# Kernel tuning notes

Measured on AMD Instinct MI355X. Metric: run time of the kernel, lower is better.

The kernel has to match this reference:

```python
import jax, jax.numpy as jnp
import numpy as np
import math

B, C, F, W, NH = 2, 8, 1024, 512, 8
HD = F // NH


def conv2d(x, w, b):
    # NCHW 3x3 same-padding conv with bias
    y = jax.lax.conv_general_dilated(x, w, (1, 1), [(1, 1), (1, 1)],
                                     dimension_numbers=('NCHW', 'OIHW', 'NCHW'))
    return y + b[None, :, None, None]


def mc_linear(x, w):
    # per-channel linear over the feature (h) axis: (b,c,h,w) x (c,f,h) -> (b,c,f,w)
    return jnp.einsum('bchw,cfh->bcfw', x, w)


def split_heads(t):
    # (b,c,f,w) -> transpose(2,3) -> (b,c,w,f) -> (b,c,w,nh,hd) -> (b,c,nh,w,hd)
    b, c, f, w = t.shape
    return jnp.transpose(t.transpose(0, 1, 3, 2).reshape(b, c, w, NH, HD), (0, 1, 3, 2, 4))


def rotate_queries_or_keys(x):
    # lucidrains-style interleaved rotary over the sequence axis (dim -2)
    d, w = x.shape[-1], x.shape[-2]
    inv_freq = 1.0 / (10000.0 ** (jnp.arange(0, d, 2, dtype=jnp.float32) / d))
    freqs = jnp.arange(w, dtype=jnp.float32)[:, None] * inv_freq[None, :]  # (w, d/2)
    freqs = jnp.repeat(freqs, 2, axis=-1)  # (w, d)
    cos, sin = jnp.cos(freqs), jnp.sin(freqs)
    xp = x.reshape(*x.shape[:-1], d // 2, 2)
    x1, x2 = xp[..., 0], xp[..., 1]
    x_rot = jnp.stack((-x2, x1), axis=-1).reshape(x.shape)
    return x * cos + x_rot * sin


def _forward(x, prev_qk, wq_conv, bq_conv, wq_lin, wk_conv, bk_conv, wk_lin,
             wv_conv, bv_conv, wv_lin, wo_lin):
    b, c, h, w = x.shape
    q = rotate_queries_or_keys(split_heads(mc_linear(conv2d(x, wq_conv, bq_conv), wq_lin)))
    k = rotate_queries_or_keys(split_heads(mc_linear(conv2d(x, wk_conv, bk_conv), wk_lin)))
    v = split_heads(mc_linear(conv2d(x, wv_conv, bv_conv), wv_lin))
    # NOTE: original scales by sqrt(h) == sqrt(features), not sqrt(head_dim)
    qk = jnp.einsum('bcnqd,bcnkd->bcnqk', q, k) / math.sqrt(h) + prev_qk
    a = jnp.einsum('bcnqk,bcnkd->bcnqd', jax.nn.softmax(qk, axis=-1), v)
    a = jnp.transpose(a, (0, 1, 3, 2, 4)).reshape(b, c, w, h).transpose(0, 1, 3, 2)
    out = mc_linear(a, wo_lin)
    return out, qk


def setup_inputs() -> dict:
    key = jax.random.key(0)
    ks = jax.random.split(key, 10)
    s = 0.02
    return {
        'x': jax.random.normal(ks[0], (B, C, F, W), dtype=jnp.float32),
        'prev_qk': jax.random.normal(ks[1], (B, C, NH, W, W), dtype=jnp.float32) * 0.1,
        'wq_conv': jax.random.normal(ks[2], (C, C, 3, 3), dtype=jnp.float32) * s,
        'bq_conv': jnp.zeros((C,), dtype=jnp.float32),
        'wq_lin': jax.random.normal(ks[3], (C, F, F), dtype=jnp.float32) * s,
        'wk_conv': jax.random.normal(ks[4], (C, C, 3, 3), dtype=jnp.float32) * s,
        'bk_conv': jnp.zeros((C,), dtype=jnp.float32),
        'wk_lin': jax.random.normal(ks[5], (C, F, F), dtype=jnp.float32) * s,
        'wv_conv': jax.random.normal(ks[6], (C, C, 3, 3), dtype=jnp.float32) * s,
        'bv_conv': jnp.zeros((C,), dtype=jnp.float32),
        'wv_lin': jax.random.normal(ks[7], (C, F, F), dtype=jnp.float32) * s,
        'wo_lin': jax.random.normal(ks[8], (C, F, F), dtype=jnp.float32) * s,
    }


def reference(x, prev_qk, wq_conv, bq_conv, wq_lin, wk_conv, bk_conv, wk_lin,
              wv_conv, bv_conv, wv_lin, wo_lin):
    return _forward(x, prev_qk, wq_conv, bq_conv, wq_lin, wk_conv, bk_conv, wk_lin,
                    wv_conv, bv_conv, wv_lin, wo_lin)
```

## Files before the change

kernel.cpp:

```cpp
#include <hip/hip_runtime.h>
#include <stdint.h>


typedef float f32x4 __attribute__((ext_vector_type(4)));
typedef short s16x8 __attribute__((ext_vector_type(8)));

__device__ __forceinline__ short f2bf(float f) {
  union { float f; uint32_t u; } v; v.f = f;
  uint32_t r = v.u + 0x7FFFu + ((v.u >> 16) & 1u);
  return (short)(r >> 16);
}

__device__ __forceinline__ void g2l16(const void* g, void* l) {
  __builtin_amdgcn_global_load_lds(
      (const __attribute__((address_space(1))) void*)g,
      (__attribute__((address_space(3))) void*)l, 16, 0, 0);
}

__device__ __forceinline__ void gemm_core(const short* __restrict__ A,
                                          const short* __restrict__ B,
                                          int K, short* sA, short* sB,
                                          f32x4 (*acc)[4]) {
  const int tid = threadIdx.x;
  const int lane = tid & 63;
  const int wv = tid >> 6;
  const int wm = wv >> 1, wn = wv & 1;
  const int q = lane >> 4, cix = lane & 15;

  for (int k0 = 0; k0 < K; k0 += 32) {
    __syncthreads();
#pragma unroll
    for (int i = 0; i < 2; ++i) {
      int seg = wv + 4 * i;
      int m = seg * 16 + (lane >> 2);
      int ko = (lane & 3) * 8;
      g2l16(B + (size_t)m * K + k0 + ko, sB + seg * 512);
    }
#pragma unroll
    for (int i = 0; i < 2; ++i) {
      int seg = wv + 4 * i;
      int m = seg * 16 + (lane >> 2);
      int ko = (lane & 3) * 8;
      g2l16(A + (size_t)m * K + k0 + ko, sA + seg * 512);
    }
    __syncthreads();
    s16x8 afr[4], bfr[4];
#pragma unroll
    for (int i = 0; i < 4; ++i)
      afr[i] = *(const s16x8*)(sA + (wm * 64 + i * 16 + cix) * 32 + q * 8);
#pragma unroll
    for (int i = 0; i < 4; ++i)
      bfr[i] = *(const s16x8*)(sB + (wn * 64 + i * 16 + cix) * 32 + q * 8);
#pragma unroll
    for (int i = 0; i < 4; ++i)
#pragma unroll
      for (int j = 0; j < 4; ++j)
        acc[i][j] = __builtin_amdgcn_mfma_f32_16x16x32_bf16(afr[i], bfr[j],
                                                            acc[i][j], 0, 0, 0);
  }
}

__global__ void __launch_bounds__(256) k_cvt(
    const float* __restrict__ w0, const float* __restrict__ w1,
    const float* __restrict__ w2, const float* __restrict__ w3,
    short* __restrict__ Wb) {
  size_t i = (size_t)blockIdx.x * 256 + threadIdx.x;
#pragma unroll
  for (int r = 0; r < 4; ++r) {
    const float* s = (r == 0) ? w0 : (r == 1) ? w1 : (r == 2) ? w2 : w3;
    size_t v = i + (size_t)r * 2097152;
    float4 f = *(const float4*)(s + (i << 2));
    short4 o;
    o.x = f2bf(f.x); o.y = f2bf(f.y); o.z = f2bf(f.z); o.w = f2bf(f.w);
    *(short4*)(Wb + (v << 2)) = o;
  }
}

__global__ void __launch_bounds__(256) k_conv(
    const float* __restrict__ x,
    const float* __restrict__ wqc, const float* __restrict__ bqc,
    const float* __restrict__ wkc, const float* __restrict__ bkc,
    const float* __restrict__ wvc, const float* __restrict__ bvc,
    short* __restrict__ Yt) {
  __shared__ float xs[8][66][19];
  const int h0 = blockIdx.x * 64, w0 = blockIdx.y * 16, b = blockIdx.z;
  const int tid = threadIdx.x;
  for (int idx = tid; idx < 8 * 66 * 18; idx += 256) {
    int c = idx / (66 * 18);
    int rem = idx % (66 * 18);
    int r = rem / 18, cc = rem % 18;
    int h = h0 + r - 1, w = w0 + cc - 1;
    float v = 0.f;
    if (h >= 0 && h < 1024 && w >= 0 && w < 512)
      v = x[(((size_t)b * 8 + c) << 10 | (unsigned)h) * 512 + w];
    xs[c][r][cc] = v;
  }
  __syncthreads();
  const int hh = tid & 63;
  const int wv4 = tid >> 6;
  const size_t hgl = h0 + hh;
  for (int proj = 0; proj < 3; ++proj) {
    const float* wc = (proj == 0) ? wqc : ((proj == 1) ? wkc : wvc);
    const float* bc = (proj == 0) ? bqc : ((proj == 1) ? bkc : bvc);
    float a[4][8];
#pragma unroll
    for (int jj = 0; jj < 4; ++jj)
#pragma unroll
      for (int co = 0; co < 8; ++co) a[jj][co] = bc[co];
    for (int ci = 0; ci < 8; ++ci)
#pragma unroll
      for (int dh = 0; dh < 3; ++dh)
#pragma unroll
        for (int dw = 0; dw < 3; ++dw) {
          float xv[4];
#pragma unroll
          for (int jj = 0; jj < 4; ++jj)
            xv[jj] = xs[ci][hh + dh][wv4 * 4 + jj + dw];
          const int wi = ci * 9 + dh * 3 + dw;
#pragma unroll
          for (int co = 0; co < 8; ++co) {
            float wgt = wc[co * 72 + wi];
#pragma unroll
            for (int jj = 0; jj < 4; ++jj) a[jj][co] = fmaf(xv[jj], wgt, a[jj][co]);
          }
        }
#pragma unroll
    for (int jj = 0; jj < 4; ++jj) {
      size_t col = (size_t)b * 512 + w0 + wv4 * 4 + jj;
#pragma unroll
      for (int co = 0; co < 8; ++co)
        Yt[((size_t)(proj * 8 + co) << 20) + (col << 10) + hgl] = f2bf(a[jj][co]);
    }
  }
}

__global__ void __launch_bounds__(256) k_qkv(
    const short* __restrict__ Wb, const short* __restrict__ Yt,
    short* __restrict__ Qr, short* __restrict__ Kr, short* __restrict__ Vt) {
  __shared__ short sA[128 * 32], sB[128 * 32];
  const int L = blockIdx.x;
  const int lin = (L & 7) * 192 + (L >> 3);
  const int g = lin >> 6;
  const int t = lin & 63;
  const int proj = g >> 3, cq = g & 7;
  const int mt = t >> 3, nt = t & 7;
  const short* A = Wb + ((size_t)g << 20) + ((size_t)mt << 17);
  const short* B = Yt + ((size_t)g << 20) + ((size_t)nt << 17);
  const f32x4 fzero = {0.f, 0.f, 0.f, 0.f};
  f32x4 acc[4][4];
#pragma unroll
  for (int i = 0; i < 4; ++i)
#pragma unroll
    for (int j = 0; j < 4; ++j) acc[i][j] = fzero;
  gemm_core(A, B, 1024, sA, sB, acc);

  const int lane = threadIdx.x & 63, wv = threadIdx.x >> 6;
  const int wm = wv >> 1, wn = wv & 1, q = lane >> 4, cix = lane & 15;
  const int head = mt;
  if (proj == 2) {
#pragma unroll
    for (int mi = 0; mi < 4; ++mi) {
      int rbase = wm * 64 + mi * 16 + q * 4;
#pragma unroll
      for (int ni = 0; ni < 4; ++ni) {
        int col = nt * 128 + wn * 64 + ni * 16 + cix;
        int b = col >> 9, wpos = col & 511;
        size_t base = ((size_t)((cq * 8 + head) * 2 + b) << 16) +
                      ((size_t)rbase << 9) + wpos;
        f32x4 v = acc[mi][ni];
        Vt[base] = f2bf(v[0]);
        Vt[base + 512] = f2bf(v[1]);
        Vt[base + 1024] = f2bf(v[2]);
        Vt[base + 1536] = f2bf(v[3]);
      }
    }
  } else {
    short* QKp = proj ? Kr : Qr;
#pragma unroll
    for (int mi = 0; mi < 4; ++mi) {
      int rbase = wm * 64 + mi * 16 + q * 4;
      int j0 = rbase >> 1;
      float if0 = exp2f(-0.20762050593046f * (float)j0);
      float if1 = exp2f(-0.20762050593046f * (float)(j0 + 1));
#pragma unroll
      for (int ni = 0; ni < 4; ++ni) {
        int col = nt * 128 + wn * 64 + ni * 16 + cix;
        int b = col >> 9, wpos = col & 511;
        float fw = (float)wpos;
        float s0, c0, s1, c1;
        __sincosf(fw * if0, &s0, &c0);
        __sincosf(fw * if1, &s1, &c1);
        f32x4 v = acc[mi][ni];
        short4 pk;
        pk.x = f2bf(v[0] * c0 - v[1] * s0);
        pk.y = f2bf(v[1] * c0 + v[0] * s0);
        pk.z = f2bf(v[2] * c1 - v[3] * s1);
        pk.w = f2bf(v[3] * c1 + v[2] * s1);
        *(short4*)&QKp[((size_t)(((cq * 8 + head) * 2 + b) * 512 + wpos) << 7) +
                       rbase] = pk;
      }
    }
  }
}

__global__ void __launch_bounds__(256, 2) k_attn(
    const short* __restrict__ Qr, const short* __restrict__ Kr,
    const short* __restrict__ Vt, const float* __restrict__ prevqk,
    float* __restrict__ qk, short* __restrict__ At) {
  __shared__ short Qs[128 * 128];
  __shared__ short Pt[128 * 136];
  __shared__ float psum[128][2];
  const int tid = threadIdx.x, lane = tid & 63, wv = tid >> 6;
  const int wm = wv >> 1, wn = wv & 1, q = lane >> 4, cix = lane & 15;
  const int qt = blockIdx.x, bcn = blockIdx.y;
  const int b = bcn >> 6, cch = (bcn >> 3) & 7, nh = bcn & 7;
  const size_t qrb = ((size_t)((cch * 8 + nh) * 2 + b)) << 16;
  const size_t rowg0 = (size_t)bcn * 512 + qt * 128;
  const int arow = wm * 64;

  {
    const char* Qg = (const char*)(Qr + qrb + ((size_t)qt << 14));
#pragma unroll
    for (int i = 0; i < 8; ++i) {
      int Lb = i * 4096 + wv * 1024;
      int L = Lb + (lane << 4);
      int src = (L & ~255) | ((L & 255) ^ (((L >> 8) & 15) << 4));
      g2l16(Qg + src, (char*)Qs + Lb);
    }
  }
  __syncthreads();

  const f32x4 fzero = {0.f, 0.f, 0.f, 0.f};
  f32x4 accO[4][4];
  float lsum[4][4];
#pragma unroll
  for (int i = 0; i < 4; ++i)
#pragma unroll
    for (int j = 0; j < 4; ++j) { accO[i][j] = fzero; lsum[i][j] = 0.f; }

  float pvA[16], pvB[16];

#pragma unroll 1
  for (int kt = 0; kt < 4; ++kt) {
    const int colb = kt * 128 + wn * 64 + cix;
    f32x4 accS[4][4];
#pragma unroll
    for (int i = 0; i < 4; ++i)
#pragma unroll
      for (int j = 0; j < 4; ++j) accS[i][j] = fzero;

#pragma unroll
    for (int ni = 0; ni < 4; ++ni)
#pragma unroll
      for (int r = 0; r < 4; ++r)
        pvA[ni * 4 + r] =
            prevqk[((rowg0 + arow + q * 4 + r) << 9) + colb + ni * 16];

    const short* Kbase = Kr + qrb + ((size_t)kt << 14);
#pragma unroll
    for (int kk = 0; kk < 4; ++kk) {
      s16x8 afr[4], bfr[4];
      const int cb = kk * 64 + q * 16;
#pragma unroll
      for (int ni = 0; ni < 4; ++ni)
        bfr[ni] = *(const s16x8*)(Kbase +
            ((size_t)(wn * 64 + ni * 16 + cix) << 7) + kk * 32 + q * 8);
#pragma unroll
      for (int mi = 0; mi < 4; ++mi) {
        const int row = arow + mi * 16 + cix;
        afr[mi] = *(const s16x8*)((const char*)Qs + row * 256 +
                                  (cb ^ ((row & 15) << 4)));
      }
#pragma unroll
      for (int mi = 0; mi < 4; ++mi)
#pragma unroll
        for (int ni = 0; ni < 4; ++ni)
          accS[mi][ni] = __builtin_amdgcn_mfma_f32_16x16x32_bf16(
              afr[mi], bfr[ni], accS[mi][ni], 0, 0, 0);
    }

    auto ldchunk = [&](int mi, float* dst) {
#pragma unroll
      for (int ni = 0; ni < 4; ++ni)
#pragma unroll
        for (int r = 0; r < 4; ++r)
          dst[ni * 4 + r] =
              prevqk[((rowg0 + arow + mi * 16 + q * 4 + r) << 9) +
                     colb + ni * 16];
    };
    auto process = [&](int mi, const float* pv) {
      float rs[4] = {0.f, 0.f, 0.f, 0.f};
#pragma unroll
      for (int ni = 0; ni < 4; ++ni)
#pragma unroll
        for (int r = 0; r < 4; ++r) {
          float s = accS[mi][ni][r] * 0.03125f + pv[ni * 4 + r];
          qk[((rowg0 + arow + mi * 16 + q * 4 + r) << 9) + colb + ni * 16] = s;
          float p = __expf(s);
          rs[r] += p;
          Pt[(arow + mi * 16 + q * 4 + r) * 136 + wn * 64 + ni * 16 + cix] =
              f2bf(p);
        }
#pragma unroll
      for (int r = 0; r < 4; ++r) lsum[mi][r] += rs[r];
    };
    ldchunk(1, pvB);
    process(0, pvA);
    ldchunk(2, pvA);
    process(1, pvB);
    ldchunk(3, pvB);
    process(2, pvA);
    process(3, pvB);

    __syncthreads();

#pragma unroll
    for (int s4 = 0; s4 < 4; ++s4) {
      s16x8 afr[4], bfr[4];
#pragma unroll
      for (int i = 0; i < 4; ++i)
        afr[i] =
            *(const s16x8*)&Pt[(arow + i * 16 + cix) * 136 + s4 * 32 + q * 8];
#pragma unroll
      for (int i = 0; i < 4; ++i)
        bfr[i] = *(const s16x8*)&Vt[qrb +
                                    ((size_t)(wn * 64 + i * 16 + cix) << 9) +
                                    kt * 128 + s4 * 32 + q * 8];
#pragma unroll
      for (int i = 0; i < 4; ++i)
#pragma unroll
        for (int j = 0; j < 4; ++j)
          accO[i][j] = __builtin_amdgcn_mfma_f32_16x16x32_bf16(
              afr[i], bfr[j], accO[i][j], 0, 0, 0);
    }
    __syncthreads();
  }

#pragma unroll
  for (int mi = 0; mi < 4; ++mi)
#pragma unroll
    for (int r = 0; r < 4; ++r) {
      float se = lsum[mi][r];
      se += __shfl_xor(se, 1);
      se += __shfl_xor(se, 2);
      se += __shfl_xor(se, 4);
      se += __shfl_xor(se, 8);
      if (cix == 0) psum[arow + mi * 16 + q * 4 + r][wn] = se;
    }
  __syncthreads();
#pragma unroll
  for (int mi = 0; mi < 4; ++mi) {
    int rl = arow + mi * 16 + q * 4;
    float iL[4];
#pragma unroll
    for (int r = 0; r < 4; ++r)
      iL[r] = 1.0f / (psum[rl + r][0] + psum[rl + r][1]);
    int wq = qt * 128 + rl;
#pragma unroll
    for (int ni = 0; ni < 4; ++ni) {
      int dl = wn * 64 + ni * 16 + cix;
      size_t ob = (((size_t)cch << 10) + b * 512 + wq) * 1024 + nh * 128 + dl;
      f32x4 v = accO[mi][ni];
      At[ob] = f2bf(v[0] * iL[0]);
      At[ob + 1024] = f2bf(v[1] * iL[1]);
      At[ob + 2048] = f2bf(v[2] * iL[2]);
      At[ob + 3072] = f2bf(v[3] * iL[3]);
    }
  }
}

__global__ void __launch_bounds__(256) k_out(
    const short* __restrict__ At, const short* __restrict__ Wob,
    float* __restrict__ outp) {
  __shared__ short sA[128 * 32], sB[128 * 32];
  const int L = blockIdx.x;
  const int lin = (L & 7) * 64 + (L >> 3);
  const int c = lin >> 6;
  const int t = lin & 63;
  const int mt = t >> 3, nt = t & 7;
  const short* A = At + ((size_t)c << 20) + ((size_t)mt << 17);
  const short* B = Wob + ((size_t)c << 20) + ((size_t)nt << 17);
  const f32x4 fzero = {0.f, 0.f, 0.f, 0.f};
  f32x4 acc[4][4];
#pragma unroll
  for (int i = 0; i < 4; ++i)
#pragma unroll
    for (int j = 0; j < 4; ++j) acc[i][j] = fzero;
  gemm_core(A, B, 1024, sA, sB, acc);

  const int lane = threadIdx.x & 63, wv = threadIdx.x >> 6;
  const int wm = wv >> 1, wn = wv & 1, q = lane >> 4, cix = lane & 15;
#pragma unroll
  for (int mi = 0; mi < 4; ++mi) {
    int colm = mt * 128 + wm * 64 + mi * 16 + q * 4;
    int b = colm >> 9, w = colm & 511;
#pragma unroll
    for (int ni = 0; ni < 4; ++ni) {
      int f = nt * 128 + wn * 64 + ni * 16 + cix;
      f32x4 v = acc[mi][ni];
      float4 st; st.x = v[0]; st.y = v[1]; st.z = v[2]; st.w = v[3];
      *(float4*)&outp[((((size_t)b * 8 + c) << 10) + f) * 512 + w] = st;
    }
  }
}

extern "C" void kernel_launch(void* const* d_in, const int* in_sizes, int n_in,
                              void* d_out, int out_size, void* d_ws,
                              size_t ws_size, hipStream_t stream) {
  const float* x = (const float*)d_in[0];
  const float* prevqk = (const float*)d_in[1];
  const float* wqc = (const float*)d_in[2];
  const float* bqc = (const float*)d_in[3];
  const float* wql = (const float*)d_in[4];
  const float* wkc = (const float*)d_in[5];
  const float* bkc = (const float*)d_in[6];
  const float* wkl = (const float*)d_in[7];
  const float* wvc = (const float*)d_in[8];
  const float* bvc = (const float*)d_in[9];
  const float* wvl = (const float*)d_in[10];
  const float* wol = (const float*)d_in[11];
  float* outp = (float*)d_out;
  float* qk = outp + 8388608;

  char* ws = (char*)d_ws;
  short* Wb = (short*)ws;
  short* Yt = (short*)(ws + 67108864);
  short* Qr = (short*)(ws + 117440512);
  short* Kr = (short*)(ws + 134217728);
  short* Vt = (short*)(ws + 150994944);
  short* At = (short*)(ws + 67108864);
  short* Wob = Wb + ((size_t)24 << 20);

  k_cvt<<<dim3(8192), 256, 0, stream>>>(wql, wkl, wvl, wol, Wb);
  k_conv<<<dim3(16, 32, 2), 256, 0, stream>>>(x, wqc, bqc, wkc, bkc, wvc, bvc, Yt);
  k_qkv<<<dim3(1536), 256, 0, stream>>>(Wb, Yt, Qr, Kr, Vt);
  k_attn<<<dim3(4, 128), 256, 0, stream>>>(Qr, Kr, Vt, prevqk, qk, At);
  k_out<<<dim3(512), 256, 0, stream>>>(At, Wob, outp);
}
```

Measured before the change: 581.9 us.

## Drop Q LDS staging in attention, raise occupancy, remap blocks, interleave loads

The attention kernel stops staging the Q tile in shared memory and reads Q fragments straight from global memory. This cuts LDS use so the launch bound can ask for three blocks per CU instead of two. The grid becomes 1D with a swizzled block-to-(head, q-tile) mapping, and prev_qk prefetch buffers shrink to half-chunks issued ahead of the first QK MMA. It also interleaves K and V fragment loads with MFMAs under raised s_setprio. The trade-off is more global traffic for Q, which is reread per kt iteration and per wave, in exchange for higher occupancy and lower register pressure.

```diff
diff --git a/kernel.cpp b/kernel.cpp
--- a/kernel.cpp
+++ b/kernel.cpp
@@ -203,32 +203,22 @@
   }
 }
 
-__global__ void __launch_bounds__(256, 2) k_attn(
+__global__ void __launch_bounds__(256, 3) k_attn(
     const short* __restrict__ Qr, const short* __restrict__ Kr,
     const short* __restrict__ Vt, const float* __restrict__ prevqk,
     float* __restrict__ qk, short* __restrict__ At) {
-  __shared__ short Qs[128 * 128];
   __shared__ short Pt[128 * 136];
   __shared__ float psum[128][2];
   const int tid = threadIdx.x, lane = tid & 63, wv = tid >> 6;
   const int wm = wv >> 1, wn = wv & 1, q = lane >> 4, cix = lane & 15;
-  const int qt = blockIdx.x, bcn = blockIdx.y;
+  const int bid = blockIdx.x;
+  const int lin = (bid & 7) * 64 + (bid >> 3);
+  const int bcn = lin >> 2, qt = lin & 3;
   const int b = bcn >> 6, cch = (bcn >> 3) & 7, nh = bcn & 7;
   const size_t qrb = ((size_t)((cch * 8 + nh) * 2 + b)) << 16;
   const size_t rowg0 = (size_t)bcn * 512 + qt * 128;
   const int arow = wm * 64;
-
-  {
-    const char* Qg = (const char*)(Qr + qrb + ((size_t)qt << 14));
-#pragma unroll
-    for (int i = 0; i < 8; ++i) {
-      int Lb = i * 4096 + wv * 1024;
-      int L = Lb + (lane << 4);
-      int src = (L & ~255) | ((L & 255) ^ (((L >> 8) & 15) << 4));
-      g2l16(Qg + src, (char*)Qs + Lb);
-    }
-  }
-  __syncthreads();
+  const short* Qbase = Qr + qrb + ((size_t)qt << 14);
 
   const f32x4 fzero = {0.f, 0.f, 0.f, 0.f};
   f32x4 accO[4][4];
@@ -238,7 +228,7 @@
 #pragma unroll
     for (int j = 0; j < 4; ++j) { accO[i][j] = fzero; lsum[i][j] = 0.f; }
 
-  float pvA[16], pvB[16];
+  float pvA[8], pvB[8];
 
 #pragma unroll 1
   for (int kt = 0; kt < 4; ++kt) {
@@ -249,89 +239,84 @@
 #pragma unroll
       for (int j = 0; j < 4; ++j) accS[i][j] = fzero;
 
-#pragma unroll
-    for (int ni = 0; ni < 4; ++ni)
-#pragma unroll
-      for (int r = 0; r < 4; ++r)
-        pvA[ni * 4 + r] =
-            prevqk[((rowg0 + arow + q * 4 + r) << 9) + colb + ni * 16];
-
-    const short* Kbase = Kr + qrb + ((size_t)kt << 14);
-#pragma unroll
-    for (int kk = 0; kk < 4; ++kk) {
-      s16x8 afr[4], bfr[4];
-      const int cb = kk * 64 + q * 16;
-#pragma unroll
-      for (int ni = 0; ni < 4; ++ni)
-        bfr[ni] = *(const s16x8*)(Kbase +
-            ((size_t)(wn * 64 + ni * 16 + cix) << 7) + kk * 32 + q * 8);
-#pragma unroll
-      for (int mi = 0; mi < 4; ++mi) {
-        const int row = arow + mi * 16 + cix;
-        afr[mi] = *(const s16x8*)((const char*)Qs + row * 256 +
-                                  (cb ^ ((row & 15) << 4)));
-      }
-#pragma unroll
-      for (int mi = 0; mi < 4; ++mi)
-#pragma unroll
-        for (int ni = 0; ni < 4; ++ni)
-          accS[mi][ni] = __builtin_amdgcn_mfma_f32_16x16x32_bf16(
-              afr[mi], bfr[ni], accS[mi][ni], 0, 0, 0);
-    }
-
-    auto ldchunk = [&](int mi, float* dst) {
-#pragma unroll
-      for (int ni = 0; ni < 4; ++ni)
+    auto ld8 = [&](int mi, int h, float* dst) {
+#pragma unroll
+      for (int u = 0; u < 2; ++u)
 #pragma unroll
         for (int r = 0; r < 4; ++r)
-          dst[ni * 4 + r] =
+          dst[u * 4 + r] =
               prevqk[((rowg0 + arow + mi * 16 + q * 4 + r) << 9) +
-                     colb + ni * 16];
+                     colb + (2 * h + u) * 16];
     };
-    auto process = [&](int mi, const float* pv) {
-      float rs[4] = {0.f, 0.f, 0.f, 0.f};
-#pragma unroll
-      for (int ni = 0; ni < 4; ++ni)
+    auto pr8 = [&](int mi, int h, const float* pv) {
+#pragma unroll
+      for (int u = 0; u < 2; ++u) {
+        int ni = 2 * h + u;
 #pragma unroll
         for (int r = 0; r < 4; ++r) {
-          float s = accS[mi][ni][r] * 0.03125f + pv[ni * 4 + r];
+          float s = accS[mi][ni][r] * 0.03125f + pv[u * 4 + r];
           qk[((rowg0 + arow + mi * 16 + q * 4 + r) << 9) + colb + ni * 16] = s;
           float p = __expf(s);
-          rs[r] += p;
+          lsum[mi][r] += p;
           Pt[(arow + mi * 16 + q * 4 + r) * 136 + wn * 64 + ni * 16 + cix] =
               f2bf(p);
         }
-#pragma unroll
-      for (int r = 0; r < 4; ++r) lsum[mi][r] += rs[r];
+      }
     };
-    ldchunk(1, pvB);
-    process(0, pvA);
-    ldchunk(2, pvA);
-    process(1, pvB);
-    ldchunk(3, pvB);
-    process(2, pvA);
-    process(3, pvB);
+
+    ld8(0, 0, pvA);
+
+    const short* Kbase = Kr + qrb + ((size_t)kt << 14);
+#pragma unroll
+    for (int kk = 0; kk < 4; ++kk) {
+      s16x8 afr[4];
+#pragma unroll
+      for (int mi = 0; mi < 4; ++mi)
+        afr[mi] = *(const s16x8*)(Qbase +
+            ((size_t)(arow + mi * 16 + cix) << 7) + kk * 32 + q * 8);
+      __builtin_amdgcn_s_setprio(1);
+#pragma unroll
+      for (int ni = 0; ni < 4; ++ni) {
+        s16x8 bfr = *(const s16x8*)(Kbase +
+            ((size_t)(wn * 64 + ni * 16 + cix) << 7) + kk * 32 + q * 8);
+#pragma unroll
+        for (int mi = 0; mi < 4; ++mi)
+          accS[mi][ni] = __builtin_amdgcn_mfma_f32_16x16x32_bf16(
+              afr[mi], bfr, accS[mi][ni], 0, 0, 0);
+      }
+      __builtin_amdgcn_s_setprio(0);
+    }
+
+    ld8(0, 1, pvB); pr8(0, 0, pvA);
+    ld8(1, 0, pvA); pr8(0, 1, pvB);
+    ld8(1, 1, pvB); pr8(1, 0, pvA);
+    ld8(2, 0, pvA); pr8(1, 1, pvB);
+    ld8(2, 1, pvB); pr8(2, 0, pvA);
+    ld8(3, 0, pvA); pr8(2, 1, pvB);
+    ld8(3, 1, pvB); pr8(3, 0, pvA);
+    pr8(3, 1, pvB);
 
     __syncthreads();
 
 #pragma unroll
     for (int s4 = 0; s4 < 4; ++s4) {
-      s16x8 afr[4], bfr[4];
+      s16x8 afr[4];
 #pragma unroll
       for (int i = 0; i < 4; ++i)
         afr[i] =
             *(const s16x8*)&Pt[(arow + i * 16 + cix) * 136 + s4 * 32 + q * 8];
-#pragma unroll
-      for (int i = 0; i < 4; ++i)
-        bfr[i] = *(const s16x8*)&Vt[qrb +
-                                    ((size_t)(wn * 64 + i * 16 + cix) << 9) +
-                                    kt * 128 + s4 * 32 + q * 8];
-#pragma unroll
-      for (int i = 0; i < 4; ++i)
-#pragma unroll
-        for (int j = 0; j < 4; ++j)
+      __builtin_amdgcn_s_setprio(1);
+#pragma unroll
+      for (int j = 0; j < 4; ++j) {
+        s16x8 bfr = *(const s16x8*)&Vt[qrb +
+                                       ((size_t)(wn * 64 + j * 16 + cix) << 9) +
+                                       kt * 128 + s4 * 32 + q * 8];
+#pragma unroll
+        for (int i = 0; i < 4; ++i)
           accO[i][j] = __builtin_amdgcn_mfma_f32_16x16x32_bf16(
-              afr[i], bfr[j], accO[i][j], 0, 0, 0);
+              afr[i], bfr, accO[i][j], 0, 0, 0);
+      }
+      __builtin_amdgcn_s_setprio(0);
     }
     __syncthreads();
   }
@@ -434,6 +419,6 @@
   k_cvt<<<dim3(8192), 256, 0, stream>>>(wql, wkl, wvl, wol, Wb);
   k_conv<<<dim3(16, 32, 2), 256, 0, stream>>>(x, wqc, bqc, wkc, bkc, wvc, bvc, Yt);
   k_qkv<<<dim3(1536), 256, 0, stream>>>(Wb, Yt, Qr, Kr, Vt);
-  k_attn<<<dim3(4, 128), 256, 0, stream>>>(Qr, Kr, Vt, prevqk, qk, At);
+  k_attn<<<dim3(512), 256, 0, stream>>>(Qr, Kr, Vt, prevqk, qk, At);
   k_out<<<dim3(512), 256, 0, stream>>>(At, Wob, outp);
 }
```

New measurement: 670.6 us. 15.2% more time.
